# Kernel optimization log

Measured on AMD Instinct MI355X. Metric: run time of the kernel, lower is better.

## Reference

```python
import jax, jax.numpy as jnp
import numpy as np
import math

B, S, D = 1, 512, 512
N = 8
DH = D // N  # 64


def setup_inputs() -> dict:
    key = jax.random.key(0)
    ks = jax.random.split(key, 12)
    s = 1.0 / math.sqrt(D)
    return {
        "hidden_states": jax.random.normal(ks[0], (B, S, D), dtype=jnp.float32),
        "attention_mask": jnp.ones((B, S), dtype=jnp.float32),
        # Linear weights stored as [in, out] (math-equivalent to torch x @ W.T + b)
        "Wq": jax.random.normal(ks[1], (D, D), dtype=jnp.float32) * s,
        "bq": jax.random.normal(ks[2], (D,), dtype=jnp.float32) * 0.01,
        "Wk": jax.random.normal(ks[3], (D, D), dtype=jnp.float32) * s,
        "bk": jax.random.normal(ks[4], (D,), dtype=jnp.float32) * 0.01,
        "Wv": jax.random.normal(ks[5], (D, D), dtype=jnp.float32) * s,
        "bv": jax.random.normal(ks[6], (D,), dtype=jnp.float32) * 0.01,
        "Wo": jax.random.normal(ks[7], (D, D), dtype=jnp.float32) * s,
        "bo": jax.random.normal(ks[8], (D,), dtype=jnp.float32) * 0.01,
        "gamma": jnp.ones((1,), dtype=jnp.float32) * math.sqrt(DH),
        "alpha": jnp.zeros((1,), dtype=jnp.float32),
    }


def _heads(x):
    # [B,S,D] -> [B,N,S,DH]
    return x.reshape(B, S, N, DH).transpose(0, 2, 1, 3)


def reference(hidden_states, attention_mask, Wq, bq, Wk, bk, Wv, bv, Wo, bo, gamma, alpha):
    q = _heads(hidden_states @ Wq + bq)  # [B,N,S,DH]
    k = _heads(hidden_states @ Wk + bk)
    v = _heads(hidden_states @ Wv + bv)

    # Manhattan-distance scores: z[b,n,i,j] = sum_d |q - k|
    abs_diff = jnp.abs(q[:, :, :, None, :] - k[:, :, None, :, :])  # [B,N,S,S,DH]
    z = abs_diff.sum(-1) / (gamma * math.sqrt(DH))  # [B,N,S,S]
    z_prime = jax.nn.relu(z - alpha)

    # mask: [B,S] -> [B,1,1,S]; masked-out keys get huge inhibition
    z_prime = z_prime + (1.0 - attention_mask)[:, None, None, :] * 1e10

    # inhibition: context[b,n,i,d] = sum_j relu(v[b,n,j,d] - z'[b,n,i,j])
    inhibited = jax.nn.relu(v[:, :, None, :, :] - z_prime[..., None])  # [B,N,S,S,DH]
    context = inhibited.sum(axis=3)  # [B,N,S,DH]  (dropout is identity at eval)

    context = context.transpose(0, 2, 1, 3).reshape(B, S, D)
    return context @ Wo + bo
```

## Files before the change

kernel.cpp:

```cpp
#include <hip/hip_runtime.h>

#define S 512
#define Dm 512

typedef __bf16 bf16x8 __attribute__((ext_vector_type(8)));
typedef float f32x4 __attribute__((ext_vector_type(4)));

__global__ __launch_bounds__(256) void prep_kernel(
    const float* __restrict__ hs,
    const float* __restrict__ W0, const float* __restrict__ W1,
    const float* __restrict__ W2, const float* __restrict__ W3,
    __bf16* __restrict__ Abf,
    __bf16* __restrict__ T0, __bf16* __restrict__ T1,
    __bf16* __restrict__ T2, __bf16* __restrict__ T3)
{
    __shared__ __bf16 Tl[64][72];
    int u = threadIdx.x;
    if (blockIdx.x < 128) {
        int i = (blockIdx.x * 256 + u) * 8;
        float4 x0 = *(const float4*)(hs + i);
        float4 x1 = *(const float4*)(hs + i + 4);
        bf16x8 y;
        y[0] = (__bf16)x0.x; y[1] = (__bf16)x0.y; y[2] = (__bf16)x0.z; y[3] = (__bf16)x0.w;
        y[4] = (__bf16)x1.x; y[5] = (__bf16)x1.y; y[6] = (__bf16)x1.z; y[7] = (__bf16)x1.w;
        *(bf16x8*)(Abf + i) = y;
        return;
    }
    int blk = blockIdx.x - 128;
    int m = blk >> 6;
    int t = blk & 63;
    const float* W = (m == 0) ? W0 : (m == 1) ? W1 : (m == 2) ? W2 : W3;
    __bf16* T = (m == 0) ? T0 : (m == 1) ? T1 : (m == 2) ? T2 : T3;
    int k0 = (t >> 3) << 6;
    int n0 = (t & 7) << 6;
    {
        int kk = u >> 4;
        int n4 = (u & 15) << 2;
        #pragma unroll
        for (int p = 0; p < 4; ++p) {
            int k = kk + (p << 4);
            float4 wv = *(const float4*)(W + (k0 + k) * Dm + n0 + n4);
            Tl[n4 + 0][k] = (__bf16)wv.x;
            Tl[n4 + 1][k] = (__bf16)wv.y;
            Tl[n4 + 2][k] = (__bf16)wv.z;
            Tl[n4 + 3][k] = (__bf16)wv.w;
        }
    }
    __syncthreads();
    {
        int n = u >> 2;
        int ks = (u & 3) << 4;
        uint4 d0 = *(const uint4*)&Tl[n][ks];
        uint4 d1 = *(const uint4*)&Tl[n][ks + 8];
        *(uint4*)(T + (n0 + n) * Dm + k0 + ks) = d0;
        *(uint4*)(T + (n0 + n) * Dm + k0 + ks + 8) = d1;
    }
}

template<bool TRANSQK>
__global__ __launch_bounds__(256) void gemm_bf(
    const __bf16* __restrict__ Abf,
    const __bf16* __restrict__ T0, const __bf16* __restrict__ T1, const __bf16* __restrict__ T2,
    const float* __restrict__ b0, const float* __restrict__ b1, const float* __restrict__ b2,
    float* __restrict__ O0, float* __restrict__ O1, float* __restrict__ O2)
{
    int blk = blockIdx.x;
    int m = blk >> 8;
    int tile = blk & 255;
    const __bf16* T = (m == 0) ? T0 : (m == 1) ? T1 : T2;
    const float* bias = (m == 0) ? b0 : (m == 1) ? b1 : b2;
    float* O = (m == 0) ? O0 : (m == 1) ? O1 : O2;
    int rt = tile >> 4, ct = tile & 15;

    int u = threadIdx.x;
    int w = u >> 6, lane = u & 63;
    int r = lane & 15, kg = lane >> 4;

    int row0 = (rt << 5) + ((w >> 1) << 4);
    int col0 = (ct << 5) + ((w & 1) << 4);

    const __bf16* Ap = Abf + (row0 + r) * Dm + (kg << 3);
    const __bf16* Bp = T + (col0 + r) * Dm + (kg << 3);

    f32x4 acc = {0.f, 0.f, 0.f, 0.f};

    #pragma unroll 4
    for (int k0 = 0; k0 < Dm; k0 += 32) {
        bf16x8 a = *(const bf16x8*)(Ap + k0);
        bf16x8 b = *(const bf16x8*)(Bp + k0);
        acc = __builtin_amdgcn_mfma_f32_16x16x32_bf16(a, b, acc, 0, 0, 0);
    }

    int orow = row0 + (kg << 2);
    float bb = bias[col0 + r];

    if constexpr (TRANSQK) {
        if (m < 2) {
            float4 o = make_float4(acc[0] + bb, acc[1] + bb, acc[2] + bb, acc[3] + bb);
            *(float4*)(O + (col0 + r) * S + orow) = o;
            return;
        }
    }
    #pragma unroll
    for (int t = 0; t < 4; ++t)
        O[(orow + t) * Dm + col0 + r] = acc[t] + bb;
}

__global__ __launch_bounds__(512) void zctx_kernel(
    const float* __restrict__ QT, const float* __restrict__ KT, const float* __restrict__ V,
    const float* __restrict__ mask, const float* __restrict__ gamma,
    const float* __restrict__ alpha, __bf16* __restrict__ ctxb)
{
    int blk = blockIdx.x;
    int h  = blk >> 6;
    int it = blk & 63;
    int i0 = it << 3;
    int c0 = h << 6;

    int u = threadIdx.x;
    int w = u >> 6, lane = u & 63;
    int jj = (w << 6) + lane;

    __shared__ float zs[8][512];
    __shared__ float zpart[8][8];
    __shared__ float part[8][8][64];

    const float* kcol = KT + (c0 * S) + jj;
    const float* qrow = QT + (c0 * S) + i0;

    float acc[8] = {};
    #pragma unroll 4
    for (int d = 0; d < 64; ++d) {
        float kv = kcol[d * S];
        float4 qa = *(const float4*)(qrow + d * S);
        float4 qb = *(const float4*)(qrow + d * S + 4);
        acc[0] += fabsf(qa.x - kv);
        acc[1] += fabsf(qa.y - kv);
        acc[2] += fabsf(qa.z - kv);
        acc[3] += fabsf(qa.w - kv);
        acc[4] += fabsf(qb.x - kv);
        acc[5] += fabsf(qb.y - kv);
        acc[6] += fabsf(qb.z - kv);
        acc[7] += fabsf(qb.w - kv);
    }

    float sc = 1.0f / (gamma[0] * 8.0f);
    float al = alpha[0];
    float madd = (1.0f - mask[jj]) * 1e6f;

    float zpv[8];
    #pragma unroll
    for (int r = 0; r < 8; ++r) {
        zpv[r] = fmaxf(acc[r] * sc - al, 0.0f) + madd;
        zs[r][jj] = zpv[r];
    }

    #pragma unroll
    for (int r = 0; r < 8; ++r) {
        float v = zpv[r];
        v += __shfl_xor(v, 1, 64);
        v += __shfl_xor(v, 2, 64);
        v += __shfl_xor(v, 4, 64);
        v += __shfl_xor(v, 8, 64);
        v += __shfl_xor(v, 16, 64);
        v += __shfl_xor(v, 32, 64);
        zpv[r] = v;
    }
    if (lane == 0) {
        #pragma unroll
        for (int r = 0; r < 8; ++r) zpart[w][r] = zpv[r];
    }
    __syncthreads();

    int wu = __builtin_amdgcn_readfirstlane(w);
    float a2[8][4] = {};

    #pragma unroll
    for (int cch = 0; cch < 4; ++cch) {
        int jg = (cch << 7) + (wu << 4);
        float vv[16];
        #pragma unroll
        for (int t = 0; t < 16; ++t)
            vv[t] = V[(jg + t) * Dm + c0 + lane];

        #pragma unroll
        for (int ii = 0; ii < 8; ++ii) {
            #pragma unroll
            for (int q4 = 0; q4 < 4; ++q4) {
                float4 z4 = *(const float4*)&zs[ii][jg + (q4 << 2)];
                a2[ii][0] += fmaxf(vv[(q4 << 2) + 0], z4.x);
                a2[ii][1] += fmaxf(vv[(q4 << 2) + 1], z4.y);
                a2[ii][2] += fmaxf(vv[(q4 << 2) + 2], z4.z);
                a2[ii][3] += fmaxf(vv[(q4 << 2) + 3], z4.w);
            }
        }
    }

    #pragma unroll
    for (int ii = 0; ii < 8; ++ii)
        part[w][ii][lane] = (a2[ii][0] + a2[ii][1]) + (a2[ii][2] + a2[ii][3]);
    __syncthreads();

    {
        int ii = u >> 6;
        float s = 0.f;
        #pragma unroll
        for (int ww = 0; ww < 8; ++ww) s += part[ww][ii][lane];
        float zsum = 0.f;
        #pragma unroll
        for (int p = 0; p < 8; ++p) zsum += zpart[p][ii];
        ctxb[(i0 + ii) * Dm + c0 + lane] = (__bf16)(s - zsum);
    }
}

extern "C" void kernel_launch(void* const* d_in, const int* in_sizes, int n_in,
                              void* d_out, int out_size, void* d_ws, size_t ws_size,
                              hipStream_t stream) {
    const float* hs    = (const float*)d_in[0];
    const float* mask  = (const float*)d_in[1];
    const float* Wq    = (const float*)d_in[2];
    const float* bq    = (const float*)d_in[3];
    const float* Wk    = (const float*)d_in[4];
    const float* bk    = (const float*)d_in[5];
    const float* Wv    = (const float*)d_in[6];
    const float* bv    = (const float*)d_in[7];
    const float* Wo    = (const float*)d_in[8];
    const float* bo    = (const float*)d_in[9];
    const float* gamma = (const float*)d_in[10];
    const float* alpha = (const float*)d_in[11];
    float* out = (float*)d_out;

    char* base = (char*)d_ws;
    float*  QT  = (float*)(base);
    float*  KT  = QT + S * Dm;
    float*  Vb  = KT + S * Dm;
    __bf16* Abf = (__bf16*)(Vb + S * Dm);
    __bf16* T0  = Abf + S * Dm;
    __bf16* T1  = T0 + S * Dm;
    __bf16* T2  = T1 + S * Dm;
    __bf16* T3  = T2 + S * Dm;
    __bf16* Cbf = T3 + S * Dm;

    hipLaunchKernelGGL(prep_kernel, dim3(384), dim3(256), 0, stream,
                       hs, Wq, Wk, Wv, Wo, Abf, T0, T1, T2, T3);
    hipLaunchKernelGGL((gemm_bf<true>), dim3(768), dim3(256), 0, stream,
                       Abf, T0, T1, T2, bq, bk, bv, QT, KT, Vb);
    hipLaunchKernelGGL(zctx_kernel, dim3(512), dim3(512), 0, stream,
                       QT, KT, Vb, mask, gamma, alpha, Cbf);
    hipLaunchKernelGGL((gemm_bf<false>), dim3(256), dim3(256), 0, stream,
                       Cbf, T3, T3, T3, bo, bo, bo, out, out, out);
}
```

Before: 54.19 us.

## Compute Manhattan scores and inhibition in packed fp16 with transposed z layout

Q, K and V are written as fp16 instead of fp32, and the L1-distance and max-accumulate loops in the attention kernel use packed half2 arithmetic (v_pk_max_f16, packed sub/add). The shared z buffer is stored as [j][8] fp16 so each key yields one 16-byte read covering all eight query rows, and z is clamped to 64 so it fits in fp16. This aims to halve memory traffic and double ALU throughput in the dominant kernel. In exchange, partial sums accumulate in fp16 across 16-element chunks and the 64-element distance, which risks accuracy loss against the fp32 reference.

New measurement: 47.02 us (median of 2 runs). -13.2%, faster.

```diff
diff --git a/kernel.cpp b/kernel.cpp
--- a/kernel.cpp
+++ b/kernel.cpp
@@ -5,6 +5,19 @@
 
 typedef __bf16 bf16x8 __attribute__((ext_vector_type(8)));
 typedef float f32x4 __attribute__((ext_vector_type(4)));
+typedef _Float16 half_t;
+typedef half_t h2 __attribute__((ext_vector_type(2)));
+typedef half_t h4 __attribute__((ext_vector_type(4)));
+
+static __device__ __forceinline__ h2 habs2(h2 x) {
+    unsigned u = __builtin_bit_cast(unsigned, x) & 0x7FFF7FFFu;
+    return __builtin_bit_cast(h2, u);
+}
+static __device__ __forceinline__ h2 hmax2(h2 a, h2 b) {
+    h2 r;
+    asm("v_pk_max_f16 %0, %1, %2" : "=v"(r) : "v"(a), "v"(b));
+    return r;
+}
 
 __global__ __launch_bounds__(256) void prep_kernel(
     const float* __restrict__ hs,
@@ -62,14 +75,14 @@
     const __bf16* __restrict__ Abf,
     const __bf16* __restrict__ T0, const __bf16* __restrict__ T1, const __bf16* __restrict__ T2,
     const float* __restrict__ b0, const float* __restrict__ b1, const float* __restrict__ b2,
-    float* __restrict__ O0, float* __restrict__ O1, float* __restrict__ O2)
+    void* __restrict__ O0, void* __restrict__ O1, void* __restrict__ O2)
 {
     int blk = blockIdx.x;
     int m = blk >> 8;
     int tile = blk & 255;
     const __bf16* T = (m == 0) ? T0 : (m == 1) ? T1 : T2;
     const float* bias = (m == 0) ? b0 : (m == 1) ? b1 : b2;
-    float* O = (m == 0) ? O0 : (m == 1) ? O1 : O2;
+    void* Ov = (m == 0) ? O0 : (m == 1) ? O1 : O2;
     int rt = tile >> 4, ct = tile & 15;
 
     int u = threadIdx.x;
@@ -96,18 +109,29 @@
 
     if constexpr (TRANSQK) {
         if (m < 2) {
-            float4 o = make_float4(acc[0] + bb, acc[1] + bb, acc[2] + bb, acc[3] + bb);
-            *(float4*)(O + (col0 + r) * S + orow) = o;
-            return;
-        }
-    }
+            half_t* O = (half_t*)Ov;
+            h4 o;
+            o[0] = (half_t)(acc[0] + bb);
+            o[1] = (half_t)(acc[1] + bb);
+            o[2] = (half_t)(acc[2] + bb);
+            o[3] = (half_t)(acc[3] + bb);
+            *(h4*)(O + (col0 + r) * S + orow) = o;
+        } else {
+            half_t* V = (half_t*)Ov;
+            #pragma unroll
+            for (int t = 0; t < 4; ++t)
+                V[(orow + t) * Dm + col0 + r] = (half_t)(acc[t] + bb);
+        }
+        return;
+    }
+    float* O = (float*)Ov;
     #pragma unroll
     for (int t = 0; t < 4; ++t)
         O[(orow + t) * Dm + col0 + r] = acc[t] + bb;
 }
 
 __global__ __launch_bounds__(512) void zctx_kernel(
-    const float* __restrict__ QT, const float* __restrict__ KT, const float* __restrict__ V,
+    const half_t* __restrict__ QT, const half_t* __restrict__ KT, const half_t* __restrict__ V,
     const float* __restrict__ mask, const float* __restrict__ gamma,
     const float* __restrict__ alpha, __bf16* __restrict__ ctxb)
 {
@@ -121,84 +145,94 @@
     int w = u >> 6, lane = u & 63;
     int jj = (w << 6) + lane;
 
-    __shared__ float zs[8][512];
+    __shared__ half_t zs[512][8];
     __shared__ float zpart[8][8];
     __shared__ float part[8][8][64];
 
-    const float* kcol = KT + (c0 * S) + jj;
-    const float* qrow = QT + (c0 * S) + i0;
-
-    float acc[8] = {};
-    #pragma unroll 4
+    const half_t* kcol = KT + (c0 * S) + jj;
+    const half_t* qrow = QT + (c0 * S) + i0;
+
+    h2 acc2[4] = {};
+    #pragma unroll 8
     for (int d = 0; d < 64; ++d) {
-        float kv = kcol[d * S];
-        float4 qa = *(const float4*)(qrow + d * S);
-        float4 qb = *(const float4*)(qrow + d * S + 4);
-        acc[0] += fabsf(qa.x - kv);
-        acc[1] += fabsf(qa.y - kv);
-        acc[2] += fabsf(qa.z - kv);
-        acc[3] += fabsf(qa.w - kv);
-        acc[4] += fabsf(qb.x - kv);
-        acc[5] += fabsf(qb.y - kv);
-        acc[6] += fabsf(qb.z - kv);
-        acc[7] += fabsf(qb.w - kv);
+        half_t kh = kcol[d * S];
+        h2 k2 = {kh, kh};
+        uint4 qu = *(const uint4*)(qrow + d * S);
+        h2 q0 = __builtin_bit_cast(h2, qu.x);
+        h2 q1 = __builtin_bit_cast(h2, qu.y);
+        h2 q2 = __builtin_bit_cast(h2, qu.z);
+        h2 q3 = __builtin_bit_cast(h2, qu.w);
+        acc2[0] += habs2(q0 - k2);
+        acc2[1] += habs2(q1 - k2);
+        acc2[2] += habs2(q2 - k2);
+        acc2[3] += habs2(q3 - k2);
     }
 
     float sc = 1.0f / (gamma[0] * 8.0f);
     float al = alpha[0];
     float madd = (1.0f - mask[jj]) * 1e6f;
 
-    float zpv[8];
+    float zrs[8];
+    h4 zlo, zhi;
+    #pragma unroll
+    for (int p = 0; p < 4; ++p) {
+        float s0 = (float)acc2[p].x;
+        float s1 = (float)acc2[p].y;
+        float z0 = fminf(fmaxf(s0 * sc - al, 0.0f) + madd, 64.0f);
+        float z1 = fminf(fmaxf(s1 * sc - al, 0.0f) + madd, 64.0f);
+        half_t h0 = (half_t)z0, h1 = (half_t)z1;
+        if (p < 2) { zlo[2 * p] = h0; zlo[2 * p + 1] = h1; }
+        else       { zhi[2 * (p - 2)] = h0; zhi[2 * (p - 2) + 1] = h1; }
+        zrs[2 * p] = (float)h0;
+        zrs[2 * p + 1] = (float)h1;
+    }
+    *(h4*)&zs[jj][0] = zlo;
+    *(h4*)&zs[jj][4] = zhi;
+
     #pragma unroll
     for (int r = 0; r < 8; ++r) {
-        zpv[r] = fmaxf(acc[r] * sc - al, 0.0f) + madd;
-        zs[r][jj] = zpv[r];
-    }
-
-    #pragma unroll
-    for (int r = 0; r < 8; ++r) {
-        float v = zpv[r];
+        float v = zrs[r];
         v += __shfl_xor(v, 1, 64);
         v += __shfl_xor(v, 2, 64);
         v += __shfl_xor(v, 4, 64);
         v += __shfl_xor(v, 8, 64);
         v += __shfl_xor(v, 16, 64);
         v += __shfl_xor(v, 32, 64);
-        zpv[r] = v;
+        zrs[r] = v;
     }
     if (lane == 0) {
         #pragma unroll
-        for (int r = 0; r < 8; ++r) zpart[w][r] = zpv[r];
+        for (int r = 0; r < 8; ++r) zpart[w][r] = zrs[r];
     }
     __syncthreads();
 
     int wu = __builtin_amdgcn_readfirstlane(w);
-    float a2[8][4] = {};
+    float accB[8] = {};
 
     #pragma unroll
     for (int cch = 0; cch < 4; ++cch) {
         int jg = (cch << 7) + (wu << 4);
-        float vv[16];
-        #pragma unroll
-        for (int t = 0; t < 16; ++t)
-            vv[t] = V[(jg + t) * Dm + c0 + lane];
-
-        #pragma unroll
-        for (int ii = 0; ii < 8; ++ii) {
-            #pragma unroll
-            for (int q4 = 0; q4 < 4; ++q4) {
-                float4 z4 = *(const float4*)&zs[ii][jg + (q4 << 2)];
-                a2[ii][0] += fmaxf(vv[(q4 << 2) + 0], z4.x);
-                a2[ii][1] += fmaxf(vv[(q4 << 2) + 1], z4.y);
-                a2[ii][2] += fmaxf(vv[(q4 << 2) + 2], z4.z);
-                a2[ii][3] += fmaxf(vv[(q4 << 2) + 3], z4.w);
-            }
+        h2 c2[4] = {};
+        #pragma unroll
+        for (int t = 0; t < 16; ++t) {
+            half_t vh = V[(jg + t) * Dm + c0 + lane];
+            h2 v2 = {vh, vh};
+            uint4 zu = *(const uint4*)&zs[jg + t][0];
+            c2[0] += hmax2(v2, __builtin_bit_cast(h2, zu.x));
+            c2[1] += hmax2(v2, __builtin_bit_cast(h2, zu.y));
+            c2[2] += hmax2(v2, __builtin_bit_cast(h2, zu.z));
+            c2[3] += hmax2(v2, __builtin_bit_cast(h2, zu.w));
+        }
+        #pragma unroll
+        for (int p = 0; p < 4; ++p) {
+            accB[2 * p]     += (float)c2[p].x;
+            accB[2 * p + 1] += (float)c2[p].y;
         }
     }
 
     #pragma unroll
     for (int ii = 0; ii < 8; ++ii)
-        part[w][ii][lane] = (a2[ii][0] + a2[ii][1]) + (a2[ii][2] + a2[ii][3]);
+        part[w][ii][lane] = accB[ii];
     __syncthreads();
 
     {
@@ -231,10 +265,10 @@
     float* out = (float*)d_out;
 
     char* base = (char*)d_ws;
-    float*  QT  = (float*)(base);
-    float*  KT  = QT + S * Dm;
-    float*  Vb  = KT + S * Dm;
-    __bf16* Abf = (__bf16*)(Vb + S * Dm);
+    half_t* QT  = (half_t*)(base);
+    half_t* KT  = QT + S * Dm;
+    half_t* V16 = KT + S * Dm;
+    __bf16* Abf = (__bf16*)(V16 + S * Dm);
     __bf16* T0  = Abf + S * Dm;
     __bf16* T1  = T0 + S * Dm;
     __bf16* T2  = T1 + S * Dm;
@@ -244,9 +278,11 @@
     hipLaunchKernelGGL(prep_kernel, dim3(384), dim3(256), 0, stream,
                        hs, Wq, Wk, Wv, Wo, Abf, T0, T1, T2, T3);
     hipLaunchKernelGGL((gemm_bf<true>), dim3(768), dim3(256), 0, stream,
-                       Abf, T0, T1, T2, bq, bk, bv, QT, KT, Vb);
+                       Abf, T0, T1, T2, bq, bk, bv,
+                       (void*)QT, (void*)KT, (void*)V16);
     hipLaunchKernelGGL(zctx_kernel, dim3(512), dim3(512), 0, stream,
-                       QT, KT, Vb, mask, gamma, alpha, Cbf);
+                       QT, KT, V16, mask, gamma, alpha, Cbf);
     hipLaunchKernelGGL((gemm_bf<false>), dim3(256), dim3(256), 0, stream,
-                       Cbf, T3, T3, T3, bo, bo, bo, out, out, out);
-}
+                       Cbf, T3, T3, T3, bo, bo, bo,
+                       (void*)out, (void*)out, (void*)out);
+}
```
